# Performance work log

Measured on AMD Instinct MI355X. Metric: run time of the kernel, lower is better.

The kernel has to match this reference:

```python
import jax, jax.numpy as jnp
import numpy as np

B, S, V, H, NH, DFF, L, T = 16, 256, 30522, 768, 12, 3072, 12, 9
DH = H // NH
LN_EPS = 1e-12


def _ln(x, g, b):
    m = x.mean(-1, keepdims=True)
    v = ((x - m) ** 2).mean(-1, keepdims=True)
    return (x - m) * jax.lax.rsqrt(v + LN_EPS) * g + b


def setup_inputs() -> dict:
    key = jax.random.key(0)
    ks = jax.random.split(key, 20)
    n = lambda k, shp: jax.random.normal(k, shp, jnp.float32) * 0.02
    return {
        "x": jax.random.randint(ks[0], (B, S), 0, V),
        "target": jax.random.randint(ks[1], (B, S), 0, T),
        "word_emb": n(ks[2], (V, H)),
        "pos_emb": n(ks[3], (S, H)),
        "type_emb": n(ks[4], (2, H)),
        "emb_ln_g": jnp.ones((H,)), "emb_ln_b": jnp.zeros((H,)),
        "Wq": n(ks[5], (L, H, H)), "bq": jnp.zeros((L, H)),
        "Wk": n(ks[6], (L, H, H)), "bk": jnp.zeros((L, H)),
        "Wv": n(ks[7], (L, H, H)), "bv": jnp.zeros((L, H)),
        "Wo": n(ks[8], (L, H, H)), "bo": jnp.zeros((L, H)),
        "ln1_g": jnp.ones((L, H)), "ln1_b": jnp.zeros((L, H)),
        "W1": n(ks[9], (L, H, DFF)), "b1": jnp.zeros((L, DFF)),
        "W2": n(ks[10], (L, DFF, H)), "b2": jnp.zeros((L, H)),
        "ln2_g": jnp.ones((L, H)), "ln2_b": jnp.zeros((L, H)),
        "clf_W": n(ks[11], (H, T)), "clf_b": jnp.zeros((T,)),
        "crf_start": jax.random.uniform(ks[12], (T,), jnp.float32, -0.1, 0.1),
        "crf_trans": jax.random.uniform(ks[13], (T, T), jnp.float32, -0.1, 0.1),
        "crf_end": jax.random.uniform(ks[14], (T,), jnp.float32, -0.1, 0.1),
    }


def _forward(x, target, word_emb, pos_emb, type_emb, emb_ln_g, emb_ln_b,
             Wq, bq, Wk, bk, Wv, bv, Wo, bo, ln1_g, ln1_b,
             W1, b1, W2, b2, ln2_g, ln2_b, clf_W, clf_b,
             crf_start, crf_trans, crf_end):
    # ---- BERT-base encoder (post-LN), no attention mask (all tokens valid) ----
    h = _ln(word_emb[x] + pos_emb[None, :, :] + type_emb[0][None, None, :], emb_ln_g, emb_ln_b)
    scale = 1.0 / np.sqrt(DH).astype(np.float32)
    for l in range(L):
        q = (h @ Wq[l] + bq[l]).reshape(B, S, NH, DH)
        k = (h @ Wk[l] + bk[l]).reshape(B, S, NH, DH)
        v = (h @ Wv[l] + bv[l]).reshape(B, S, NH, DH)
        att = jax.nn.softmax(jnp.einsum('bqhd,bkhd->bhqk', q, k) * scale, axis=-1)
        ctx = jnp.einsum('bhqk,bkhd->bqhd', att, v).reshape(B, S, H)
        h = _ln(h + ctx @ Wo[l] + bo[l], ln1_g[l], ln1_b[l])
        ff = jax.nn.gelu(h @ W1[l] + b1[l], approximate=False) @ W2[l] + b2[l]
        h = _ln(h + ff, ln2_g[l], ln2_b[l])

    logits = h @ clf_W + clf_b  # [B,S,T] emissions

    # ---- CRF negative log-likelihood (torchcrf semantics, reduction='mean') ----
    mask = target > -1                      # [B,S] bool
    tags = jnp.where(mask, target, 0)
    bidx = jnp.arange(B)
    emit = jnp.take_along_axis(logits, tags[..., None], axis=-1)[..., 0]  # [B,S]

    # numerator: score of the gold path
    num = crf_start[tags[:, 0]] + emit[:, 0]
    trans = crf_trans[tags[:, :-1], tags[:, 1:]]                          # [B,S-1]
    num = num + jnp.sum((trans + emit[:, 1:]) * mask[:, 1:], axis=1)
    last = jnp.sum(mask.astype(jnp.int32), axis=1) - 1
    num = num + crf_end[tags[bidx, last]]

    # denominator: forward algorithm (logsumexp recurrence over time)
    alpha0 = crf_start[None, :] + logits[:, 0]                            # [B,T]

    def step(alpha, xs):
        em, m = xs                                                        # [B,T], [B]
        nxt = jax.nn.logsumexp(alpha[:, :, None] + crf_trans[None], axis=1) + em
        return jnp.where(m[:, None], nxt, alpha), None

    alpha, _ = jax.lax.scan(step, alpha0,
                            (jnp.swapaxes(logits[:, 1:], 0, 1),
                             jnp.swapaxes(mask[:, 1:], 0, 1)))
    denom = jax.nn.logsumexp(alpha + crf_end[None, :], axis=1)

    llh = num - denom
    return -jnp.mean(llh)  # model returns -loss where loss = mean log-likelihood


def reference(x, target, word_emb, pos_emb, type_emb, emb_ln_g, emb_ln_b,
              Wq, bq, Wk, bk, Wv, bv, Wo, bo, ln1_g, ln1_b,
              W1, b1, W2, b2, ln2_g, ln2_b, clf_W, clf_b,
              crf_start, crf_trans, crf_end):
    return _forward(x, target, word_emb, pos_emb, type_emb, emb_ln_g, emb_ln_b,
                    Wq, bq, Wk, bk, Wv, bv, Wo, bo, ln1_g, ln1_b,
                    W1, b1, W2, b2, ln2_g, ln2_b, clf_W, clf_b,
                    crf_start, crf_trans, crf_end)
```

## Files before the change

kernel.cpp:

```cpp
#include <hip/hip_runtime.h>
#include <math.h>

#define B 16
#define S 256
#define H 768
#define NH 12
#define DH 64
#define DFF 3072
#define L 12
#define T 9
#define M (B*S)
#define LN_EPS 1e-12f
#define QKVS (3*H)
#define NCH 16

typedef __attribute__((ext_vector_type(8))) __bf16 bf16x8;
typedef __attribute__((ext_vector_type(8))) unsigned short u16x8;
typedef __attribute__((ext_vector_type(4))) unsigned short u16x4;
typedef __attribute__((ext_vector_type(4))) float f32x4;

__device__ __forceinline__ unsigned short f2bf(float f) {
    unsigned int u = __float_as_uint(f);
    unsigned int r = u + 0x7fffu + ((u >> 16) & 1u);
    return (unsigned short)(r >> 16);
}
__device__ __forceinline__ float bf2f(unsigned short h) {
    return __uint_as_float((unsigned int)h << 16);
}

__global__ void convT_kernel(const float* __restrict__ W, unsigned short* __restrict__ WT,
                             int K, int N, size_t dstLayerStride) {
    __shared__ float tile[32][33];
    const int layer = blockIdx.z;
    const float* Wp = W + (size_t)layer * K * N;
    unsigned short* Tp = WT + (size_t)layer * dstLayerStride;
    const int n0 = blockIdx.x * 32, k0 = blockIdx.y * 32;
    const int tx = threadIdx.x, ty = threadIdx.y;
#pragma unroll
    for (int i = 0; i < 32; i += 8)
        tile[ty + i][tx] = Wp[(size_t)(k0 + ty + i) * N + n0 + tx];
    __syncthreads();
    {
        const int u = ty * 32 + tx;
        const int r = u >> 3, kq = (u & 7) << 2;
        u16x4 o;
#pragma unroll
        for (int j = 0; j < 4; ++j) o[j] = f2bf(tile[kq + j][r]);
        *(u16x4*)&Tp[(size_t)(n0 + r) * K + k0 + kq] = o;
    }
}

__global__ void biascat_kernel(const float* __restrict__ bq, const float* __restrict__ bk,
                               const float* __restrict__ bv, float* __restrict__ out) {
    int idx = blockIdx.x * 256 + threadIdx.x;
    if (idx >= L * QKVS) return;
    int l = idx / QKVS, c = idx % QKVS;
    float v = (c < H) ? bq[l * H + c] : (c < 2 * H) ? bk[l * H + c - H] : bv[l * H + c - 2 * H];
    out[idx] = v;
}

__global__ void embed_ln_kernel(const int* __restrict__ x,
                                const float* __restrict__ word_emb,
                                const float* __restrict__ pos_emb,
                                const float* __restrict__ type_emb,
                                const float* __restrict__ g,
                                const float* __restrict__ bta,
                                float* __restrict__ h,
                                unsigned short* __restrict__ hb) {
    const int row = blockIdx.x;
    const int s = row % S;
    const int tok = x[row];
    const int t = threadIdx.x;
    const int c = t << 2;
    const float4 wv = *(const float4*)&word_emb[(size_t)tok * H + c];
    const float4 pv = *(const float4*)&pos_emb[s * H + c];
    const float4 tv = *(const float4*)&type_emb[c];
    float v[4] = {wv.x + pv.x + tv.x, wv.y + pv.y + tv.y, wv.z + pv.z + tv.z, wv.w + pv.w + tv.w};
    float s1 = v[0] + v[1] + v[2] + v[3];
    float s2 = v[0]*v[0] + v[1]*v[1] + v[2]*v[2] + v[3]*v[3];
#pragma unroll
    for (int o = 32; o; o >>= 1) { s1 += __shfl_xor(s1, o); s2 += __shfl_xor(s2, o); }
    __shared__ float ws[3][2];
    const int w = t >> 6, l = t & 63;
    if (l == 0) { ws[w][0] = s1; ws[w][1] = s2; }
    __syncthreads();
    const float S1 = ws[0][0] + ws[1][0] + ws[2][0];
    const float S2 = ws[0][1] + ws[1][1] + ws[2][1];
    const float mean = S1 * (1.0f / H);
    const float var = fmaxf(S2 * (1.0f / H) - mean * mean, 0.f);
    const float inv = rsqrtf(var + LN_EPS);
    const float4 gv = *(const float4*)&g[c];
    const float4 bv = *(const float4*)&bta[c];
    float4 outv;
    outv.x = (v[0] - mean) * inv * gv.x + bv.x;
    outv.y = (v[1] - mean) * inv * gv.y + bv.y;
    outv.z = (v[2] - mean) * inv * gv.z + bv.z;
    outv.w = (v[3] - mean) * inv * gv.w + bv.w;
    *(float4*)&h[(size_t)row * H + c] = outv;
    u16x4 ob = {f2bf(outv.x), f2bf(outv.y), f2bf(outv.z), f2bf(outv.w)};
    *(u16x4*)&hb[(size_t)row * H + c] = ob;
}

__global__ void residual_ln_kernel(float* __restrict__ h,
                                   const float* __restrict__ delta,
                                   const float* __restrict__ g,
                                   const float* __restrict__ bta,
                                   unsigned short* __restrict__ hb) {
    const int row = blockIdx.x;
    const int t = threadIdx.x;
    const int c = t << 2;
    const float4 hv = *(const float4*)&h[(size_t)row * H + c];
    const float4 dv = *(const float4*)&delta[(size_t)row * H + c];
    float v[4] = {hv.x + dv.x, hv.y + dv.y, hv.z + dv.z, hv.w + dv.w};
    float s1 = v[0] + v[1] + v[2] + v[3];
    float s2 = v[0]*v[0] + v[1]*v[1] + v[2]*v[2] + v[3]*v[3];
#pragma unroll
    for (int o = 32; o; o >>= 1) { s1 += __shfl_xor(s1, o); s2 += __shfl_xor(s2, o); }
    __shared__ float ws[3][2];
    const int w = t >> 6, l = t & 63;
    if (l == 0) { ws[w][0] = s1; ws[w][1] = s2; }
    __syncthreads();
    const float S1 = ws[0][0] + ws[1][0] + ws[2][0];
    const float S2 = ws[0][1] + ws[1][1] + ws[2][1];
    const float mean = S1 * (1.0f / H);
    const float var = fmaxf(S2 * (1.0f / H) - mean * mean, 0.f);
    const float inv = rsqrtf(var + LN_EPS);
    const float4 gv = *(const float4*)&g[c];
    const float4 bv = *(const float4*)&bta[c];
    float4 outv;
    outv.x = (v[0] - mean) * inv * gv.x + bv.x;
    outv.y = (v[1] - mean) * inv * gv.y + bv.y;
    outv.z = (v[2] - mean) * inv * gv.z + bv.z;
    outv.w = (v[3] - mean) * inv * gv.w + bv.w;
    *(float4*)&h[(size_t)row * H + c] = outv;
    u16x4 ob = {f2bf(outv.x), f2bf(outv.y), f2bf(outv.z), f2bf(outv.w)};
    *(u16x4*)&hb[(size_t)row * H + c] = ob;
}

#define LSTR 72

template<int ACT, int WF, int WB, int MR>
__global__ __launch_bounds__(256, (MR == 2 ? 3 : 2))
void gemm_bf16(const unsigned short* __restrict__ A,
               const unsigned short* __restrict__ WT,
               const float* __restrict__ bias,
               float* __restrict__ Cf,
               unsigned short* __restrict__ Cb,
               int K, int N) {
    __shared__ unsigned short lA[MR * 32 * LSTR];
    __shared__ unsigned short lB[128 * LSTR];
    const int tid = threadIdx.x;
    const int m0 = blockIdx.y * (MR * 32), n0 = blockIdx.x << 7;
    const int l = tid & 63, w = tid >> 6;
    const int wr = w >> 1, wc = w & 1;
    const int lr = l & 15, kg = l >> 4;

    const int srow = tid >> 3, scol = (tid & 7) << 3;
    const unsigned short* gA = A + (size_t)(m0 + srow) * K + scol;
    const unsigned short* gB = WT + (size_t)(n0 + srow) * K + scol;

    f32x4 acc[MR][4];
#pragma unroll
    for (int i = 0; i < MR; ++i)
#pragma unroll
        for (int j = 0; j < 4; ++j) acc[i][j] = (f32x4){0.f, 0.f, 0.f, 0.f};

    u16x8 ra[MR], rb[4];
#pragma unroll
    for (int p = 0; p < MR; ++p) ra[p] = *(const u16x8*)(gA + (size_t)p * 32 * K);
#pragma unroll
    for (int p = 0; p < 4; ++p) rb[p] = *(const u16x8*)(gB + (size_t)p * 32 * K);

    for (int kt = 0; kt < K; kt += 64) {
#pragma unroll
        for (int p = 0; p < MR; ++p)
            *(u16x8*)&lA[(srow + p * 32) * LSTR + scol] = ra[p];
#pragma unroll
        for (int p = 0; p < 4; ++p)
            *(u16x8*)&lB[(srow + p * 32) * LSTR + scol] = rb[p];
        __syncthreads();
        if (kt + 64 < K) {
#pragma unroll
            for (int p = 0; p < MR; ++p) ra[p] = *(const u16x8*)(gA + (size_t)p * 32 * K + kt + 64);
#pragma unroll
            for (int p = 0; p < 4; ++p) rb[p] = *(const u16x8*)(gB + (size_t)p * 32 * K + kt + 64);
        }
#pragma unroll
        for (int ks = 0; ks < 2; ++ks) {
            bf16x8 af[MR], bfr[4];
#pragma unroll
            for (int m = 0; m < MR; ++m)
                af[m] = *(const bf16x8*)&lA[(wr * (MR * 16) + (m << 4) + lr) * LSTR + ks * 32 + (kg << 3)];
#pragma unroll
            for (int n = 0; n < 4; ++n)
                bfr[n] = *(const bf16x8*)&lB[((wc << 6) + (n << 4) + lr) * LSTR + ks * 32 + (kg << 3)];
#pragma unroll
            for (int m = 0; m < MR; ++m)
#pragma unroll
                for (int n = 0; n < 4; ++n)
                    acc[m][n] = __builtin_amdgcn_mfma_f32_16x16x32_bf16(af[m], bfr[n], acc[m][n], 0, 0, 0);
        }
        __syncthreads();
    }

    const int rbase = m0 + wr * (MR * 16) + (kg << 2);
    const int cbase = n0 + (wc << 6) + lr;
#pragma unroll
    for (int m = 0; m < MR; ++m) {
#pragma unroll
        for (int n = 0; n < 4; ++n) {
            const int col = cbase + (n << 4);
            const float bv = bias[col];
#pragma unroll
            for (int j = 0; j < 4; ++j) {
                const int row = rbase + (m << 4) + j;
                float v = acc[m][n][j] + bv;
                if (ACT == 1) v = 0.5f * v * (1.0f + erff(v * 0.70710678118654752440f));
                if (WF) Cf[(size_t)row * N + col] = v;
                if (WB) Cb[(size_t)row * N + col] = f2bf(v);
            }
        }
    }
}

__global__ void vtrans_kernel(const unsigned short* __restrict__ qkv,
                              unsigned short* __restrict__ vtg) {
    __shared__ unsigned short tile[64 * 264];
    const int bh = blockIdx.x;
    const int b = bh / NH, hh = bh % NH;
    const int t = threadIdx.x;
    {
        const int d0 = (t & 7) << 3;
        int s = t >> 3;
#pragma unroll
        for (int it = 0; it < 8; ++it, s += 32) {
            u16x8 v = *(const u16x8*)&qkv[(size_t)(b * S + s) * QKVS + 2 * H + hh * 64 + d0];
#pragma unroll
            for (int j = 0; j < 8; ++j) {
                int d = d0 + j;
                tile[d * 264 + (s ^ (((d >> 3) & 7) << 3))] = v[j];
            }
        }
    }
    __syncthreads();
    {
        const int s0 = (t & 31) << 3;
        int d = t >> 5;
#pragma unroll
        for (int it = 0; it < 8; ++it, d += 8) {
            int sp = s0 ^ (((d >> 3) & 7) << 3);
            u16x8 v = *(const u16x8*)&tile[d * 264 + sp];
            *(u16x8*)&vtg[(size_t)bh * (64 * 256) + d * 256 + s0] = v;
        }
    }
}

__global__ __launch_bounds__(256, 2)
void attn_mfma(const unsigned short* __restrict__ qkv,
               const unsigned short* __restrict__ vtg,
               unsigned short* __restrict__ ctxb) {
    __shared__ unsigned short Ks[256 * 72];
    __shared__ unsigned short Vt[64 * 264];
    __shared__ unsigned short Ps[4][16 * 72];

    const int blk = blockIdx.x;
    const int qc = blk & 3;
    const int hh = (blk >> 2) % NH;
    const int b = blk / (4 * NH);
    const int t = threadIdx.x;
    const int l = t & 63, w = t >> 6;
    const int l15 = l & 15, g = l >> 4;

    {
        const int c0 = (t & 7) << 3;
        int r = t >> 3;
#pragma unroll
        for (int it = 0; it < 8; ++it, r += 32) {
            u16x8 kv = *(const u16x8*)&qkv[(size_t)(b * S + r) * QKVS + H + hh * 64 + c0];
            *(u16x8*)&Ks[r * 72 + c0] = kv;
        }
    }
    {
        const int s0 = (t & 31) << 3;
        int d = t >> 5;
#pragma unroll
        for (int it = 0; it < 8; ++it, d += 8) {
            u16x8 vv = *(const u16x8*)&vtg[(size_t)(blk >> 2) * (64 * 256) + d * 256 + s0];
            *(u16x8*)&Vt[d * 264 + s0] = vv;
        }
    }
    const int qrow = qc * 64 + w * 16 + l15;
    const unsigned short* qp = &qkv[(size_t)(b * S + qrow) * QKVS + hh * 64 + g * 8];
    bf16x8 aq0 = *(const bf16x8*)qp;
    bf16x8 aq1 = *(const bf16x8*)(qp + 32);
    __syncthreads();

    f32x4 acc[16];
#pragma unroll
    for (int n = 0; n < 16; ++n) acc[n] = (f32x4){0.f, 0.f, 0.f, 0.f};
#pragma unroll
    for (int n = 0; n < 16; ++n) {
        const unsigned short* kp = &Ks[(n * 16 + l15) * 72 + g * 8];
        bf16x8 b0 = *(const bf16x8*)kp;
        bf16x8 b1 = *(const bf16x8*)(kp + 32);
        acc[n] = __builtin_amdgcn_mfma_f32_16x16x32_bf16(aq0, b0, acc[n], 0, 0, 0);
        acc[n] = __builtin_amdgcn_mfma_f32_16x16x32_bf16(aq1, b1, acc[n], 0, 0, 0);
    }

    float inv[4];
#pragma unroll
    for (int j = 0; j < 4; ++j) {
        float mx = acc[0][j];
#pragma unroll
        for (int n = 1; n < 16; ++n) mx = fmaxf(mx, acc[n][j]);
        mx = fmaxf(mx, __shfl_xor(mx, 1));
        mx = fmaxf(mx, __shfl_xor(mx, 2));
        mx = fmaxf(mx, __shfl_xor(mx, 4));
        mx = fmaxf(mx, __shfl_xor(mx, 8));
        float sum = 0.f;
#pragma unroll
        for (int n = 0; n < 16; ++n) {
            float e = exp2f((acc[n][j] - mx) * 0.18033688011112042f);
            acc[n][j] = e;
            sum += e;
        }
        sum += __shfl_xor(sum, 1);
        sum += __shfl_xor(sum, 2);
        sum += __shfl_xor(sum, 4);
        sum += __shfl_xor(sum, 8);
        inv[j] = 1.0f / sum;
    }

    f32x4 cacc[4];
#pragma unroll
    for (int nd = 0; nd < 4; ++nd) cacc[nd] = (f32x4){0.f, 0.f, 0.f, 0.f};
    unsigned short* ps = Ps[w];
#pragma unroll
    for (int c = 0; c < 4; ++c) {
#pragma unroll
        for (int nl = 0; nl < 4; ++nl) {
            int n = c * 4 + nl;
#pragma unroll
            for (int j = 0; j < 4; ++j)
                ps[(g * 4 + j) * 72 + nl * 16 + l15] = f2bf(acc[n][j]);
        }
        bf16x8 pa0 = *(const bf16x8*)&ps[l15 * 72 + g * 8];
        bf16x8 pa1 = *(const bf16x8*)&ps[l15 * 72 + 32 + g * 8];
#pragma unroll
        for (int nd = 0; nd < 4; ++nd) {
            const unsigned short* vp = &Vt[(nd * 16 + l15) * 264 + c * 64 + g * 8];
            bf16x8 v0 = *(const bf16x8*)vp;
            bf16x8 v1 = *(const bf16x8*)(vp + 32);
            cacc[nd] = __builtin_amdgcn_mfma_f32_16x16x32_bf16(pa0, v0, cacc[nd], 0, 0, 0);
            cacc[nd] = __builtin_amdgcn_mfma_f32_16x16x32_bf16(pa1, v1, cacc[nd], 0, 0, 0);
        }
    }

#pragma unroll
    for (int nd = 0; nd < 4; ++nd)
#pragma unroll
        for (int j = 0; j < 4; ++j) {
            int qr = qc * 64 + w * 16 + g * 4 + j;
            ctxb[(size_t)(b * S + qr) * H + hh * 64 + nd * 16 + l15] = f2bf(cacc[nd][j] * inv[j]);
        }
}

__global__ void clf_kernel(const float* __restrict__ h,
                           const float* __restrict__ W,
                           const float* __restrict__ bias,
                           float* __restrict__ logits) {
    const int row = blockIdx.x * 4 + (threadIdx.x >> 6);
    const int l = threadIdx.x & 63;
    const float* hp = h + (size_t)row * H;
    float acc[T] = {};
#pragma unroll
    for (int i = 0; i < 12; ++i) {
        const int k = l + (i << 6);
        const float x = hp[k];
        const float* wp = &W[k * T];
#pragma unroll
        for (int n = 0; n < T; ++n) acc[n] += x * wp[n];
    }
#pragma unroll
    for (int o = 32; o; o >>= 1)
#pragma unroll
        for (int n = 0; n < T; ++n) acc[n] += __shfl_xor(acc[n], o);
    if (l < T) logits[(size_t)row * T + l] = acc[l] + bias[l];
}

__global__ void crf_chunk_kernel(const float* __restrict__ logits,
                                 const int* __restrict__ target,
                                 const float* __restrict__ trans,
                                 float* __restrict__ Tc) {
    const int blk = blockIdx.x;
    const int b = blk >> 4, c = blk & 15;
    const int t = threadIdx.x;
    const int i = t / 9, j = t - i * 9;
    const bool act = t < 81;
    __shared__ float Tb[2][81];
    const float* lg = logits + (size_t)b * S * T;
    const int* tg = target + b * S;
    const float K2 = 1.44269504088896340736f;
    const float IK = 0.69314718055994530942f;

    float trc[T];
    if (act) {
#pragma unroll
        for (int k = 0; k < T; ++k) trc[k] = trans[k * T + j];
        Tb[0][t] = (i == j) ? 0.f : -1e30f;
    }
    __syncthreads();

    int p = 0;
    const int s0 = c * 16 + 1;
    const int s1 = (c == 15) ? S : (s0 + 16);
    for (int s = s0; s < s1; ++s) {
        if (tg[s] > -1) {
            if (act) {
                const float em = lg[s * T + j];
                float v[T];
#pragma unroll
                for (int k = 0; k < T; ++k) v[k] = Tb[p][i * 9 + k] + trc[k];
                float mx = fmaxf(v[0], v[1]);
                mx = fmaxf(mx, fmaxf(v[2], v[3]));
                mx = fmaxf(mx, fmaxf(v[4], v[5]));
                mx = fmaxf(mx, fmaxf(v[6], v[7]));
                mx = fmaxf(mx, v[8]);
                float sum = 0.f;
#pragma unroll
                for (int k = 0; k < T; ++k) sum += exp2f((v[k] - mx) * K2);
                Tb[p ^ 1][t] = mx + IK * log2f(sum) + em;
            }
            __syncthreads();
            p ^= 1;
        }
    }
    if (act) Tc[(size_t)blk * 81 + t] = Tb[p][t];
}

__global__ void crf_final_kernel(const float* __restrict__ logits,
                                 const int* __restrict__ target,
                                 const float* __restrict__ start,
                                 const float* __restrict__ trans,
                                 const float* __restrict__ endv,
                                 const float* __restrict__ Tc,
                                 float* __restrict__ llh) {
    const int b = blockIdx.x;
    const int l = threadIdx.x;
    const float* lg = logits + (size_t)b * S * T;
    const int* tg = target + b * S;
    const float K2 = 1.44269504088896340736f;
    const float IK = 0.69314718055994530942f;

    float pnum = 0.f; int pcnt = 0;
#pragma unroll
    for (int c = 0; c < 4; ++c) {
        const int s = 1 + l + (c << 6);
        if (s < S) {
            const int tcur = tg[s], tprev = tg[s - 1];
            const bool m = tcur > -1;
            const int tag = m ? tcur : 0;
            const int ptag = (tprev > -1) ? tprev : 0;
            if (m) { pnum += trans[ptag * T + tag] + lg[s * T + tag]; pcnt += 1; }
        }
    }
#pragma unroll
    for (int o = 32; o; o >>= 1) { pnum += __shfl_xor(pnum, o); pcnt += __shfl_xor(pcnt, o); }

    const int jj = (l < T) ? l : 0;
    float a = start[jj] + lg[jj];
    for (int c = 0; c < NCH; ++c) {
        const float* Tm = Tc + ((size_t)(b * NCH + c)) * 81;
        float v[T];
#pragma unroll
        for (int i2 = 0; i2 < T; ++i2) v[i2] = __shfl(a, i2) + Tm[i2 * 9 + jj];
        float mx = fmaxf(v[0], v[1]);
        mx = fmaxf(mx, fmaxf(v[2], v[3]));
        mx = fmaxf(mx, fmaxf(v[4], v[5]));
        mx = fmaxf(mx, fmaxf(v[6], v[7]));
        mx = fmaxf(mx, v[8]);
        float sum = 0.f;
#pragma unroll
        for (int k = 0; k < T; ++k) sum += exp2f((v[k] - mx) * K2);
        a = mx + IK * log2f(sum);
    }

    float val = (l < T) ? (a + endv[jj]) : -1e30f;
    float mx = val;
#pragma unroll
    for (int o = 8; o; o >>= 1) mx = fmaxf(mx, __shfl_xor(mx, o));
    float sm = (l < T) ? exp2f((val - mx) * K2) : 0.f;
#pragma unroll
    for (int o = 8; o; o >>= 1) sm += __shfl_xor(sm, o);
    const float denom = mx + IK * log2f(sm);

    if (l == 0) {
        const bool m0 = tg[0] > -1;
        const int tag0 = m0 ? tg[0] : 0;
        const int cnt = pcnt + (m0 ? 1 : 0);
        int lastIdx = cnt - 1; if (lastIdx < 0) lastIdx = 0;
        const int lt = tg[lastIdx];
        const int lastTag = (lt > -1) ? lt : 0;
        const float num = start[tag0] + lg[tag0] + pnum + endv[lastTag];
        llh[b] = num - denom;
    }
}

__global__ void crf_sum_kernel(const float* __restrict__ llh, float* __restrict__ out) {
    const int l = threadIdx.x;
    float v = (l < B) ? llh[l] : 0.f;
#pragma unroll
    for (int o = 8; o; o >>= 1) v += __shfl_xor(v, o);
    if (l == 0) out[0] = -v * (1.0f / B);
}

extern "C" void kernel_launch(void* const* d_in, const int* in_sizes, int n_in,
                              void* d_out, int out_size, void* d_ws, size_t ws_size,
                              hipStream_t stream) {
    const int*   x        = (const int*)d_in[0];
    const int*   target   = (const int*)d_in[1];
    const float* word_emb = (const float*)d_in[2];
    const float* pos_emb  = (const float*)d_in[3];
    const float* type_emb = (const float*)d_in[4];
    const float* emb_ln_g = (const float*)d_in[5];
    const float* emb_ln_b = (const float*)d_in[6];
    const float* Wq = (const float*)d_in[7];
    const float* bq = (const float*)d_in[8];
    const float* Wk = (const float*)d_in[9];
    const float* bk = (const float*)d_in[10];
    const float* Wv = (const float*)d_in[11];
    const float* bv = (const float*)d_in[12];
    const float* Wo = (const float*)d_in[13];
    const float* bo = (const float*)d_in[14];
    const float* ln1_g = (const float*)d_in[15];
    const float* ln1_b = (const float*)d_in[16];
    const float* W1 = (const float*)d_in[17];
    const float* b1 = (const float*)d_in[18];
    const float* W2 = (const float*)d_in[19];
    const float* b2 = (const float*)d_in[20];
    const float* ln2_g = (const float*)d_in[21];
    const float* ln2_b = (const float*)d_in[22];
    const float* clf_W = (const float*)d_in[23];
    const float* clf_b = (const float*)d_in[24];
    const float* crf_start = (const float*)d_in[25];
    const float* crf_trans = (const float*)d_in[26];
    const float* crf_end   = (const float*)d_in[27];

    char* ws = (char*)d_ws;
    size_t off = 0;
    auto alloc = [&](size_t bytes) { void* p = ws + off; off += (bytes + 255) & ~255ull; return p; };

    unsigned short* wqkvT = (unsigned short*)alloc((size_t)L * 3 * H * H * 2);
    unsigned short* woT   = (unsigned short*)alloc((size_t)L * H * H * 2);
    unsigned short* w1T   = (unsigned short*)alloc((size_t)L * H * DFF * 2);
    unsigned short* w2T   = (unsigned short*)alloc((size_t)L * H * DFF * 2);
    float*          bcat  = (float*)alloc((size_t)L * QKVS * 4);
    float*          h     = (float*)alloc((size_t)M * H * 4);
    unsigned short* hb    = (unsigned short*)alloc((size_t)M * H * 2);
    unsigned short* qkvb  = (unsigned short*)alloc((size_t)M * QKVS * 2);
    unsigned short* vtg   = (unsigned short*)alloc((size_t)B * NH * DH * S * 2);
    unsigned short* ctxb  = (unsigned short*)alloc((size_t)M * H * 2);
    float*          go    = (float*)alloc((size_t)M * H * 4);
    unsigned short* ffb   = (unsigned short*)alloc((size_t)M * DFF * 2);
    float*          logits = (float*)alloc((size_t)M * T * 4);
    float*          Tcbuf  = (float*)alloc((size_t)B * NCH * 81 * 4);
    float*          llh    = (float*)alloc((size_t)B * 4);

    dim3 tb(32, 8);
    convT_kernel<<<dim3(H / 32, H / 32, L), tb, 0, stream>>>(Wq, wqkvT,             H, H, (size_t)3 * H * H);
    convT_kernel<<<dim3(H / 32, H / 32, L), tb, 0, stream>>>(Wk, wqkvT + H * H,     H, H, (size_t)3 * H * H);
    convT_kernel<<<dim3(H / 32, H / 32, L), tb, 0, stream>>>(Wv, wqkvT + 2 * H * H, H, H, (size_t)3 * H * H);
    convT_kernel<<<dim3(H / 32, H / 32, L), tb, 0, stream>>>(Wo, woT, H, H, (size_t)H * H);
    convT_kernel<<<dim3(DFF / 32, H / 32, L), tb, 0, stream>>>(W1, w1T, H, DFF, (size_t)H * DFF);
    convT_kernel<<<dim3(H / 32, DFF / 32, L), tb, 0, stream>>>(W2, w2T, DFF, H, (size_t)H * DFF);
    biascat_kernel<<<(L * QKVS + 255) / 256, 256, 0, stream>>>(bq, bk, bv, bcat);

    embed_ln_kernel<<<M, 192, 0, stream>>>(x, word_emb, pos_emb, type_emb, emb_ln_g, emb_ln_b, h, hb);

    const dim3 gQKV(QKVS / 128, M / 128);
    const dim3 gH64(H / 128, M / 64);
    const dim3 gFF(DFF / 128, M / 128);

    for (int l = 0; l < L; ++l) {
        gemm_bf16<0, 0, 1, 4><<<gQKV, 256, 0, stream>>>(hb, wqkvT + (size_t)l * 3 * H * H, bcat + l * QKVS,
                                                        nullptr, qkvb, H, QKVS);
        vtrans_kernel<<<B * NH, 256, 0, stream>>>(qkvb, vtg);
        attn_mfma<<<B * NH * 4, 256, 0, stream>>>(qkvb, vtg, ctxb);
        gemm_bf16<0, 1, 0, 2><<<gH64, 256, 0, stream>>>(ctxb, woT + (size_t)l * H * H, bo + l * H, go, nullptr, H, H);
        residual_ln_kernel<<<M, 192, 0, stream>>>(h, go, ln1_g + l * H, ln1_b + l * H, hb);
        gemm_bf16<1, 0, 1, 4><<<gFF, 256, 0, stream>>>(hb, w1T + (size_t)l * H * DFF, b1 + l * DFF, nullptr, ffb, H, DFF);
        gemm_bf16<0, 1, 0, 2><<<gH64, 256, 0, stream>>>(ffb, w2T + (size_t)l * H * DFF, b2 + l * H, go, nullptr, DFF, H);
        residual_ln_kernel<<<M, 192, 0, stream>>>(h, go, ln2_g + l * H, ln2_b + l * H, hb);
    }

    clf_kernel<<<M / 4, 256, 0, stream>>>(h, clf_W, clf_b, logits);
    crf_chunk_kernel<<<B * NCH, 128, 0, stream>>>(logits, target, crf_trans, Tcbuf);
    crf_final_kernel<<<B, 64, 0, stream>>>(logits, target, crf_start, crf_trans, crf_end, Tcbuf, llh);
    crf_sum_kernel<<<1, 64, 0, stream>>>(llh, (float*)d_out);
}
```

Before: 2.005 ms.

## Fuse V transpose into attention kernel, process two query chunks per block, merge CRF reduction

Removes the separate V-transpose kernel: each attention block now loads V straight from the QKV buffer and transposes it into a swizzled shared-memory tile. Each block handles two 64-row query chunks, so K/V staging is shared across 128 queries and the grid is halved. MFMA sections are wrapped in s_setprio hints. The CRF final and sum kernels are merged into one 1024-thread block that reduces through shared memory, which drops launches but halves attention parallelism (384 blocks) and serialises the two query chunks inside each block.

```diff
diff --git a/kernel.cpp b/kernel.cpp
--- a/kernel.cpp
+++ b/kernel.cpp
@@ -223,50 +223,17 @@
     }
 }
 
-__global__ void vtrans_kernel(const unsigned short* __restrict__ qkv,
-                              unsigned short* __restrict__ vtg) {
-    __shared__ unsigned short tile[64 * 264];
-    const int bh = blockIdx.x;
-    const int b = bh / NH, hh = bh % NH;
-    const int t = threadIdx.x;
-    {
-        const int d0 = (t & 7) << 3;
-        int s = t >> 3;
-#pragma unroll
-        for (int it = 0; it < 8; ++it, s += 32) {
-            u16x8 v = *(const u16x8*)&qkv[(size_t)(b * S + s) * QKVS + 2 * H + hh * 64 + d0];
-#pragma unroll
-            for (int j = 0; j < 8; ++j) {
-                int d = d0 + j;
-                tile[d * 264 + (s ^ (((d >> 3) & 7) << 3))] = v[j];
-            }
-        }
-    }
-    __syncthreads();
-    {
-        const int s0 = (t & 31) << 3;
-        int d = t >> 5;
-#pragma unroll
-        for (int it = 0; it < 8; ++it, d += 8) {
-            int sp = s0 ^ (((d >> 3) & 7) << 3);
-            u16x8 v = *(const u16x8*)&tile[d * 264 + sp];
-            *(u16x8*)&vtg[(size_t)bh * (64 * 256) + d * 256 + s0] = v;
-        }
-    }
-}
-
 __global__ __launch_bounds__(256, 2)
 void attn_mfma(const unsigned short* __restrict__ qkv,
-               const unsigned short* __restrict__ vtg,
                unsigned short* __restrict__ ctxb) {
     __shared__ unsigned short Ks[256 * 72];
     __shared__ unsigned short Vt[64 * 264];
     __shared__ unsigned short Ps[4][16 * 72];
 
     const int blk = blockIdx.x;
-    const int qc = blk & 3;
-    const int hh = (blk >> 2) % NH;
-    const int b = blk / (4 * NH);
+    const int half = blk & 1;
+    const int hh = (blk >> 1) % NH;
+    const int b = blk / (2 * NH);
     const int t = threadIdx.x;
     const int l = t & 63, w = t >> 6;
     const int l15 = l & 15, g = l >> 4;
@@ -281,88 +248,103 @@
         }
     }
     {
-        const int s0 = (t & 31) << 3;
-        int d = t >> 5;
-#pragma unroll
-        for (int it = 0; it < 8; ++it, d += 8) {
-            u16x8 vv = *(const u16x8*)&vtg[(size_t)(blk >> 2) * (64 * 256) + d * 256 + s0];
-            *(u16x8*)&Vt[d * 264 + s0] = vv;
-        }
-    }
-    const int qrow = qc * 64 + w * 16 + l15;
-    const unsigned short* qp = &qkv[(size_t)(b * S + qrow) * QKVS + hh * 64 + g * 8];
-    bf16x8 aq0 = *(const bf16x8*)qp;
-    bf16x8 aq1 = *(const bf16x8*)(qp + 32);
+        const int d0 = (t & 7) << 3;
+        int s = t >> 3;
+#pragma unroll
+        for (int it = 0; it < 8; ++it, s += 32) {
+            u16x8 vv = *(const u16x8*)&qkv[(size_t)(b * S + s) * QKVS + 2 * H + hh * 64 + d0];
+#pragma unroll
+            for (int j = 0; j < 8; ++j) {
+                int d = d0 + j;
+                Vt[d * 264 + (s ^ (((d >> 3) & 7) << 3))] = vv[j];
+            }
+        }
+    }
     __syncthreads();
 
-    f32x4 acc[16];
-#pragma unroll
-    for (int n = 0; n < 16; ++n) acc[n] = (f32x4){0.f, 0.f, 0.f, 0.f};
-#pragma unroll
-    for (int n = 0; n < 16; ++n) {
-        const unsigned short* kp = &Ks[(n * 16 + l15) * 72 + g * 8];
-        bf16x8 b0 = *(const bf16x8*)kp;
-        bf16x8 b1 = *(const bf16x8*)(kp + 32);
-        acc[n] = __builtin_amdgcn_mfma_f32_16x16x32_bf16(aq0, b0, acc[n], 0, 0, 0);
-        acc[n] = __builtin_amdgcn_mfma_f32_16x16x32_bf16(aq1, b1, acc[n], 0, 0, 0);
-    }
-
-    float inv[4];
-#pragma unroll
-    for (int j = 0; j < 4; ++j) {
-        float mx = acc[0][j];
-#pragma unroll
-        for (int n = 1; n < 16; ++n) mx = fmaxf(mx, acc[n][j]);
-        mx = fmaxf(mx, __shfl_xor(mx, 1));
-        mx = fmaxf(mx, __shfl_xor(mx, 2));
-        mx = fmaxf(mx, __shfl_xor(mx, 4));
-        mx = fmaxf(mx, __shfl_xor(mx, 8));
-        float sum = 0.f;
+    unsigned short* ps = Ps[w];
+#pragma unroll
+    for (int qi = 0; qi < 2; ++qi) {
+        const int qrow = half * 128 + qi * 64 + w * 16 + l15;
+        const unsigned short* qp = &qkv[(size_t)(b * S + qrow) * QKVS + hh * 64 + g * 8];
+        bf16x8 aq0 = *(const bf16x8*)qp;
+        bf16x8 aq1 = *(const bf16x8*)(qp + 32);
+
+        f32x4 acc[16];
+#pragma unroll
+        for (int n = 0; n < 16; ++n) acc[n] = (f32x4){0.f, 0.f, 0.f, 0.f};
+        __builtin_amdgcn_s_setprio(1);
 #pragma unroll
         for (int n = 0; n < 16; ++n) {
-            float e = exp2f((acc[n][j] - mx) * 0.18033688011112042f);
-            acc[n][j] = e;
-            sum += e;
-        }
-        sum += __shfl_xor(sum, 1);
-        sum += __shfl_xor(sum, 2);
-        sum += __shfl_xor(sum, 4);
-        sum += __shfl_xor(sum, 8);
-        inv[j] = 1.0f / sum;
-    }
-
-    f32x4 cacc[4];
-#pragma unroll
-    for (int nd = 0; nd < 4; ++nd) cacc[nd] = (f32x4){0.f, 0.f, 0.f, 0.f};
-    unsigned short* ps = Ps[w];
-#pragma unroll
-    for (int c = 0; c < 4; ++c) {
-#pragma unroll
-        for (int nl = 0; nl < 4; ++nl) {
-            int n = c * 4 + nl;
-#pragma unroll
-            for (int j = 0; j < 4; ++j)
-                ps[(g * 4 + j) * 72 + nl * 16 + l15] = f2bf(acc[n][j]);
-        }
-        bf16x8 pa0 = *(const bf16x8*)&ps[l15 * 72 + g * 8];
-        bf16x8 pa1 = *(const bf16x8*)&ps[l15 * 72 + 32 + g * 8];
-#pragma unroll
-        for (int nd = 0; nd < 4; ++nd) {
-            const unsigned short* vp = &Vt[(nd * 16 + l15) * 264 + c * 64 + g * 8];
-            bf16x8 v0 = *(const bf16x8*)vp;
-            bf16x8 v1 = *(const bf16x8*)(vp + 32);
-            cacc[nd] = __builtin_amdgcn_mfma_f32_16x16x32_bf16(pa0, v0, cacc[nd], 0, 0, 0);
-            cacc[nd] = __builtin_amdgcn_mfma_f32_16x16x32_bf16(pa1, v1, cacc[nd], 0, 0, 0);
-        }
-    }
-
-#pragma unroll
-    for (int nd = 0; nd < 4; ++nd)
+            const unsigned short* kp = &Ks[(n * 16 + l15) * 72 + g * 8];
+            bf16x8 b0 = *(const bf16x8*)kp;
+            bf16x8 b1 = *(const bf16x8*)(kp + 32);
+            acc[n] = __builtin_amdgcn_mfma_f32_16x16x32_bf16(aq0, b0, acc[n], 0, 0, 0);
+            acc[n] = __builtin_amdgcn_mfma_f32_16x16x32_bf16(aq1, b1, acc[n], 0, 0, 0);
+        }
+        __builtin_amdgcn_s_setprio(0);
+
+        float inv[4];
 #pragma unroll
         for (int j = 0; j < 4; ++j) {
-            int qr = qc * 64 + w * 16 + g * 4 + j;
-            ctxb[(size_t)(b * S + qr) * H + hh * 64 + nd * 16 + l15] = f2bf(cacc[nd][j] * inv[j]);
-        }
+            float mx = acc[0][j];
+#pragma unroll
+            for (int n = 1; n < 16; ++n) mx = fmaxf(mx, acc[n][j]);
+            mx = fmaxf(mx, __shfl_xor(mx, 1));
+            mx = fmaxf(mx, __shfl_xor(mx, 2));
+            mx = fmaxf(mx, __shfl_xor(mx, 4));
+            mx = fmaxf(mx, __shfl_xor(mx, 8));
+            float sum = 0.f;
+#pragma unroll
+            for (int n = 0; n < 16; ++n) {
+                float e = exp2f((acc[n][j] - mx) * 0.18033688011112042f);
+                acc[n][j] = e;
+                sum += e;
+            }
+            sum += __shfl_xor(sum, 1);
+            sum += __shfl_xor(sum, 2);
+            sum += __shfl_xor(sum, 4);
+            sum += __shfl_xor(sum, 8);
+            inv[j] = 1.0f / sum;
+        }
+
+        f32x4 cacc[4];
+#pragma unroll
+        for (int nd = 0; nd < 4; ++nd) cacc[nd] = (f32x4){0.f, 0.f, 0.f, 0.f};
+#pragma unroll
+        for (int c = 0; c < 4; ++c) {
+#pragma unroll
+            for (int nl = 0; nl < 4; ++nl) {
+                int n = c * 4 + nl;
+#pragma unroll
+                for (int j = 0; j < 4; ++j)
+                    ps[(g * 4 + j) * 72 + nl * 16 + l15] = f2bf(acc[n][j]);
+            }
+            bf16x8 pa0 = *(const bf16x8*)&ps[l15 * 72 + g * 8];
+            bf16x8 pa1 = *(const bf16x8*)&ps[l15 * 72 + 32 + g * 8];
+            __builtin_amdgcn_s_setprio(1);
+#pragma unroll
+            for (int nd = 0; nd < 4; ++nd) {
+                const int d = nd * 16 + l15;
+                const int swz = ((d >> 3) & 7) << 3;
+                const unsigned short* vp0 = &Vt[d * 264 + ((c * 64 + g * 8) ^ swz)];
+                const unsigned short* vp1 = &Vt[d * 264 + ((c * 64 + 32 + g * 8) ^ swz)];
+                bf16x8 v0 = *(const bf16x8*)vp0;
+                bf16x8 v1 = *(const bf16x8*)vp1;
+                cacc[nd] = __builtin_amdgcn_mfma_f32_16x16x32_bf16(pa0, v0, cacc[nd], 0, 0, 0);
+                cacc[nd] = __builtin_amdgcn_mfma_f32_16x16x32_bf16(pa1, v1, cacc[nd], 0, 0, 0);
+            }
+            __builtin_amdgcn_s_setprio(0);
+        }
+
+#pragma unroll
+        for (int nd = 0; nd < 4; ++nd)
+#pragma unroll
+            for (int j = 0; j < 4; ++j) {
+                int qr = half * 128 + qi * 64 + w * 16 + g * 4 + j;
+                ctxb[(size_t)(b * S + qr) * H + hh * 64 + nd * 16 + l15] = f2bf(cacc[nd][j] * inv[j]);
+            }
+    }
 }
 
 __global__ void clf_kernel(const float* __restrict__ h,
@@ -438,15 +420,16 @@
     if (act) Tc[(size_t)blk * 81 + t] = Tb[p][t];
 }
 
-__global__ void crf_final_kernel(const float* __restrict__ logits,
-                                 const int* __restrict__ target,
-                                 const float* __restrict__ start,
-                                 const float* __restrict__ trans,
-                                 const float* __restrict__ endv,
-                                 const float* __restrict__ Tc,
-                                 float* __restrict__ llh) {
-    const int b = blockIdx.x;
-    const int l = threadIdx.x;
+__global__ __launch_bounds__(1024)
+void crf_final_kernel(const float* __restrict__ logits,
+                      const int* __restrict__ target,
+                      const float* __restrict__ start,
+                      const float* __restrict__ trans,
+                      const float* __restrict__ endv,
+                      const float* __restrict__ Tc,
+                      float* __restrict__ out) {
+    const int t = threadIdx.x;
+    const int b = t >> 6, l = t & 63;
     const float* lg = logits + (size_t)b * S * T;
     const int* tg = target + b * S;
     const float K2 = 1.44269504088896340736f;
@@ -494,6 +477,7 @@
     for (int o = 8; o; o >>= 1) sm += __shfl_xor(sm, o);
     const float denom = mx + IK * log2f(sm);
 
+    __shared__ float part[16];
     if (l == 0) {
         const bool m0 = tg[0] > -1;
         const int tag0 = m0 ? tg[0] : 0;
@@ -502,16 +486,15 @@
         const int lt = tg[lastIdx];
         const int lastTag = (lt > -1) ? lt : 0;
         const float num = start[tag0] + lg[tag0] + pnum + endv[lastTag];
-        llh[b] = num - denom;
-    }
-}
-
-__global__ void crf_sum_kernel(const float* __restrict__ llh, float* __restrict__ out) {
-    const int l = threadIdx.x;
-    float v = (l < B) ? llh[l] : 0.f;
-#pragma unroll
-    for (int o = 8; o; o >>= 1) v += __shfl_xor(v, o);
-    if (l == 0) out[0] = -v * (1.0f / B);
+        part[b] = num - denom;
+    }
+    __syncthreads();
+    if (t == 0) {
+        float s = 0.f;
+#pragma unroll
+        for (int i = 0; i < 16; ++i) s += part[i];
+        out[0] = -s * (1.0f / 16.0f);
+    }
 }
 
 extern "C" void kernel_launch(void* const* d_in, const int* in_sizes, int n_in,
@@ -558,13 +541,11 @@
     float*          h     = (float*)alloc((size_t)M * H * 4);
     unsigned short* hb    = (unsigned short*)alloc((size_t)M * H * 2);
     unsigned short* qkvb  = (unsigned short*)alloc((size_t)M * QKVS * 2);
-    unsigned short* vtg   = (unsigned short*)alloc((size_t)B * NH * DH * S * 2);
     unsigned short* ctxb  = (unsigned short*)alloc((size_t)M * H * 2);
     float*          go    = (float*)alloc((size_t)M * H * 4);
     unsigned short* ffb   = (unsigned short*)alloc((size_t)M * DFF * 2);
     float*          logits = (float*)alloc((size_t)M * T * 4);
     float*          Tcbuf  = (float*)alloc((size_t)B * NCH * 81 * 4);
-    float*          llh    = (float*)alloc((size_t)B * 4);
 
     dim3 tb(32, 8);
     convT_kernel<<<dim3(H / 32, H / 32, L), tb, 0, stream>>>(Wq, wqkvT,             H, H, (size_t)3 * H * H);
@@ -584,8 +565,7 @@
     for (int l = 0; l < L; ++l) {
         gemm_bf16<0, 0, 1, 4><<<gQKV, 256, 0, stream>>>(hb, wqkvT + (size_t)l * 3 * H * H, bcat + l * QKVS,
                                                         nullptr, qkvb, H, QKVS);
-        vtrans_kernel<<<B * NH, 256, 0, stream>>>(qkvb, vtg);
-        attn_mfma<<<B * NH * 4, 256, 0, stream>>>(qkvb, vtg, ctxb);
+        attn_mfma<<<B * NH * 2, 256, 0, stream>>>(qkvb, ctxb);
         gemm_bf16<0, 1, 0, 2><<<gH64, 256, 0, stream>>>(ctxb, woT + (size_t)l * H * H, bo + l * H, go, nullptr, H, H);
         residual_ln_kernel<<<M, 192, 0, stream>>>(h, go, ln1_g + l * H, ln1_b + l * H, hb);
         gemm_bf16<1, 0, 1, 4><<<gFF, 256, 0, stream>>>(hb, w1T + (size_t)l * H * DFF, b1 + l * DFF, nullptr, ffb, H, DFF);
@@ -595,6 +575,5 @@
 
     clf_kernel<<<M / 4, 256, 0, stream>>>(h, clf_W, clf_b, logits);
     crf_chunk_kernel<<<B * NCH, 128, 0, stream>>>(logits, target, crf_trans, Tcbuf);
-    crf_final_kernel<<<B, 64, 0, stream>>>(logits, target, crf_start, crf_trans, crf_end, Tcbuf, llh);
-    crf_sum_kernel<<<1, 64, 0, stream>>>(llh, (float*)d_out);
-}
+    crf_final_kernel<<<1, 1024, 0, stream>>>(logits, target, crf_start, crf_trans, crf_end, Tcbuf, (float*)d_out);
+}
```

Measured after the change: 1.964 ms. 1.02x faster.
